# Optimization experiments

Measured on AMD Instinct MI355X. Metric: run time of the kernel, lower is better.

Reference implementation:

```python
import jax, jax.numpy as jnp
import numpy as np


def setup_inputs() -> dict:
    key = jax.random.key(0)
    kq, kk, kv = jax.random.split(key, 3)
    B, H, S, D = 2, 8, 2048, 64
    Q = jax.random.normal(kq, (B, H, S, D), dtype=jnp.float32)
    K = jax.random.normal(kk, (B, 1, S, D), dtype=jnp.float32)
    V = jax.random.normal(kv, (B, 1, S, D), dtype=jnp.float32)
    return {"Q": Q, "K": K, "V": V}


def reference(Q, K, V):
    # Multi-query attention: K/V have a single shared head.
    D = Q.shape[-1]
    scale = 1.0 / jnp.sqrt(jnp.asarray(D, dtype=Q.dtype))
    Kh = K[:, 0]  # [B, S, D]
    Vh = V[:, 0]  # [B, S, D]
    # scores: [B, H, Sq, Sk]
    scores = jnp.einsum('bhqd,bkd->bhqk', Q, Kh) * scale
    probs = jax.nn.softmax(scores, axis=-1)
    out = jnp.einsum('bhqk,bkd->bhqd', probs, Vh)  # [B, H, S, D]
    return out
```

## Files before the change

### kernel.cpp

```cpp
#include <hip/hip_runtime.h>
#include <stdint.h>

typedef __attribute__((ext_vector_type(8)))  short    bf16x8;
typedef __attribute__((ext_vector_type(16))) float    f32x16;
typedef __attribute__((ext_vector_type(4)))  float    float4v;
typedef __attribute__((ext_vector_type(4)))  unsigned uint4v;

#define DEVINL static __device__ __forceinline__

#define B_  2
#define H_  8
#define S_  2048
#define D_  64
#define KVB 128
#define NKT (S_ / KVB)

DEVINL unsigned short f2bf(float f) {
  union { float f; unsigned u; } v; v.f = f;
  unsigned r = v.u + 0x7FFFu + ((v.u >> 16) & 1u);
  return (unsigned short)(r >> 16);
}

DEVINL unsigned pk2(float a, float b) {
  return (unsigned)f2bf(a) | ((unsigned)f2bf(b) << 16);
}

DEVINL void gload_lds16(const void* g, void* l) {
  __builtin_amdgcn_global_load_lds(
      (const __attribute__((address_space(1))) void*)g,
      (__attribute__((address_space(3))) void*)l, 16, 0, 0);
}

DEVINL bf16x8 frag_from_words(unsigned a, unsigned b, unsigned c, unsigned d) {
  union { unsigned u[4]; bf16x8 v; } x;
  x.u[0] = a; x.u[1] = b; x.u[2] = c; x.u[3] = d;
  return x.v;
}

#define CROW(r, hi) (((r) & 3) + 8 * ((r) >> 2) + 4 * (hi))

__global__ __launch_bounds__(256) void prep_kernel(
    const float* __restrict__ K, const float* __restrict__ V,
    unsigned short* __restrict__ Kb, unsigned short* __restrict__ Vt) {
  const int t = threadIdx.x;
  if (blockIdx.x < 128) {
    const int base = blockIdx.x * 2048 + t * 8;
    const float4v a = *(const float4v*)(K + base);
    const float4v b = *(const float4v*)(K + base + 4);
    uint4v o;
    o.x = (unsigned)f2bf(a.x) | ((unsigned)f2bf(a.y) << 16);
    o.y = (unsigned)f2bf(a.z) | ((unsigned)f2bf(a.w) << 16);
    o.z = (unsigned)f2bf(b.x) | ((unsigned)f2bf(b.y) << 16);
    o.w = (unsigned)f2bf(b.z) | ((unsigned)f2bf(b.w) << 16);
    *(uint4v*)(Kb + base) = o;
  } else {
    __shared__ float Vf[64][65];
    const int vb   = blockIdx.x - 128;
    const int b    = vb >> 5;
    const int sblk = vb & 31;
    const int r = t >> 2, c = t & 3;
    const float* src = V + ((size_t)(b * S_ + sblk * 64 + r)) * 64 + c * 16;
#pragma unroll
    for (int j = 0; j < 4; ++j) {
      float4v x = *(const float4v*)(src + 4 * j);
      Vf[r][c * 16 + 4 * j + 0] = x.x;
      Vf[r][c * 16 + 4 * j + 1] = x.y;
      Vf[r][c * 16 + 4 * j + 2] = x.z;
      Vf[r][c * 16 + 4 * j + 3] = x.w;
    }
    __syncthreads();
    unsigned short o[16];
#pragma unroll
    for (int j = 0; j < 16; ++j) o[j] = f2bf(Vf[c * 16 + j][r]);
    unsigned short* dst = Vt + ((size_t)(b * 64 + r)) * S_ + sblk * 64 + c * 16;
    uint4v w0, w1;
    w0.x = (unsigned)o[0]  | ((unsigned)o[1]  << 16);
    w0.y = (unsigned)o[2]  | ((unsigned)o[3]  << 16);
    w0.z = (unsigned)o[4]  | ((unsigned)o[5]  << 16);
    w0.w = (unsigned)o[6]  | ((unsigned)o[7]  << 16);
    w1.x = (unsigned)o[8]  | ((unsigned)o[9]  << 16);
    w1.y = (unsigned)o[10] | ((unsigned)o[11] << 16);
    w1.z = (unsigned)o[12] | ((unsigned)o[13] << 16);
    w1.w = (unsigned)o[14] | ((unsigned)o[15] << 16);
    *(uint4v*)(dst)     = w0;
    *(uint4v*)(dst + 8) = w1;
  }
}

__global__ __launch_bounds__(256, 2) void attn_kernel(
    const float* __restrict__ Q, const unsigned short* __restrict__ Kb,
    const unsigned short* __restrict__ Vt, float* __restrict__ O) {
  __shared__ __align__(16) unsigned char smem[65536];

  const int bid = blockIdx.x;
  const int b  = bid >> 8;
  const int h  = (bid >> 5) & 7;
  const int qt = bid & 31;

  const int tid  = threadIdx.x;
  const int lane = tid & 63;
  const int wave = tid >> 6;
  const int qg   = wave & 1;
  const int kh   = wave >> 1;
  const int hi   = lane >> 5;
  const int lq   = lane & 31;
  const int l7   = lane & 7;

  const unsigned short* Kbase = Kb + (size_t)b * (S_ * 64);
  const unsigned short* Vbase = Vt + (size_t)b * (64 * S_);

  const float qscale = 0.125f * 1.4426950408889634f;
  const float* qrow = Q + ((size_t)((b * H_ + h) * S_) + (size_t)(qt * 64 + qg * 32 + lq)) * 64;
  bf16x8 qfrag[4];
#pragma unroll
  for (int ks = 0; ks < 4; ++ks) {
    const float* p = qrow + ks * 16 + hi * 8;
    float4v x0 = *(const float4v*)(p);
    float4v x1 = *(const float4v*)(p + 4);
    bf16x8 f;
    f[0] = (short)f2bf(x0.x * qscale); f[1] = (short)f2bf(x0.y * qscale);
    f[2] = (short)f2bf(x0.z * qscale); f[3] = (short)f2bf(x0.w * qscale);
    f[4] = (short)f2bf(x1.x * qscale); f[5] = (short)f2bf(x1.y * qscale);
    f[6] = (short)f2bf(x1.z * qscale); f[7] = (short)f2bf(x1.w * qscale);
    qfrag[ks] = f;
  }

  const int krow   = lane >> 3;
  const int kchunk = (lane & 7) ^ krow;
  const int vrow   = lane >> 4;

  f32x16 acc0, acc1;
#pragma unroll
  for (int r = 0; r < 16; ++r) { acc0[r] = 0.f; acc1[r] = 0.f; }
  float mrun = -__builtin_inff();
  float lrun = 0.f;

#define KL(BUF) ((unsigned short*)(smem + (BUF) * 16384))
#define VL(BUF) ((unsigned short*)(smem + 32768 + (BUF) * 16384))

#define STAGE(BUF, KT)                                                                   \
  do {                                                                                   \
    _Pragma("unroll")                                                                    \
    for (int i = 0; i < 4; ++i) {                                                        \
      const int kj = wave * 4 + i;                           \
      gload_lds16(Kbase + (size_t)((KT) * KVB + kj * 8 + krow) * 64 + kchunk * 8,        \
                  KL(BUF) + kj * 512 + lane * 8);                                        \
      const int vj = wave * 4 + i;                         \
      const int vr = vj * 4 + vrow;                                                      \
      const int vch = (lane & 15) ^ (vr & 7);                                            \
      gload_lds16(Vbase + (size_t)vr * S_ + (KT) * KVB + vch * 8,                        \
                  VL(BUF) + vj * 512 + lane * 8);                                        \
    }                                                                                    \
  } while (0)

  STAGE(0, 0);

  int buf = 0;
  for (int kt = 0; kt < NKT; ++kt) {
    __syncthreads();

    if (kt + 1 < NKT) STAGE(buf ^ 1, kt + 1);

    f32x16 c0, c1;
#pragma unroll
    for (int r = 0; r < 16; ++r) { c0[r] = 0.f; c1[r] = 0.f; }
    const unsigned short* Kt = KL(buf);
    __builtin_amdgcn_s_setprio(1);
#pragma unroll
    for (int ks = 0; ks < 4; ++ks) {
      const int ch = (2 * ks + hi) ^ l7;
      const bf16x8 a0 = *(const bf16x8*)(Kt + (kh * 64 + lq) * 64 + ch * 8);
      c0 = __builtin_amdgcn_mfma_f32_32x32x16_bf16(a0, qfrag[ks], c0, 0, 0, 0);
      const bf16x8 a1 = *(const bf16x8*)(Kt + (kh * 64 + 32 + lq) * 64 + ch * 8);
      c1 = __builtin_amdgcn_mfma_f32_32x32x16_bf16(a1, qfrag[ks], c1, 0, 0, 0);
    }
    __builtin_amdgcn_s_setprio(0);

    float mx = fmaxf(c0[0], c0[1]);
#pragma unroll
    for (int r = 2; r < 16; ++r) mx = fmaxf(mx, c0[r]);
#pragma unroll
    for (int r = 0; r < 16; ++r) mx = fmaxf(mx, c1[r]);
    mx = fmaxf(mx, __shfl_xor(mx, 32));

    if (!__all(mx <= mrun + 8.f)) {
      const float mnew = fmaxf(mrun, mx);
      const float fac  = __builtin_amdgcn_exp2f(mrun - mnew);
#pragma unroll
      for (int r = 0; r < 16; ++r) {
        const float fr = __shfl(fac, CROW(r, hi));
        acc0[r] *= fr; acc1[r] *= fr;
      }
      lrun *= fac;
      mrun = mnew;
    }

    float psum = 0.f;
#pragma unroll
    for (int r = 0; r < 16; ++r) {
      c0[r] = __builtin_amdgcn_exp2f(c0[r] - mrun);
      c1[r] = __builtin_amdgcn_exp2f(c1[r] - mrun);
      psum += c0[r] + c1[r];
    }
    psum += __shfl_xor(psum, 32);
    lrun += psum;

    const unsigned short* Vb = VL(buf);
#pragma unroll
    for (int ks = 0; ks < 4; ++ks) {
      const int e = ks & 1;
      const f32x16 ct = (ks >> 1) ? c1 : c0;
      const unsigned wx0 = pk2(ct[8 * e + 0], ct[8 * e + 1]);
      const unsigned wx1 = pk2(ct[8 * e + 2], ct[8 * e + 3]);
      const unsigned wy0 = pk2(ct[8 * e + 4], ct[8 * e + 5]);
      const unsigned wy1 = pk2(ct[8 * e + 6], ct[8 * e + 7]);
      const unsigned s0 = hi ? wx0 : wy0;
      const unsigned s1 = hi ? wx1 : wy1;
      const unsigned r0 = (unsigned)__shfl_xor((int)s0, 32);
      const unsigned r1 = (unsigned)__shfl_xor((int)s1, 32);
      const bf16x8 pfrag = frag_from_words(hi ? r0 : wx0, hi ? r1 : wx1,
                                           hi ? wy0 : r0, hi ? wy1 : r1);
      const int ch = (kh * 8) | ((2 * ks + hi) ^ l7);
      __builtin_amdgcn_s_setprio(1);
      const bf16x8 bv0 = *(const bf16x8*)(Vb + (size_t)lq * 128 + ch * 8);
      acc0 = __builtin_amdgcn_mfma_f32_32x32x16_bf16(pfrag, bv0, acc0, 0, 0, 0);
      const bf16x8 bv1 = *(const bf16x8*)(Vb + (size_t)(32 + lq) * 128 + ch * 8);
      acc1 = __builtin_amdgcn_mfma_f32_32x32x16_bf16(pfrag, bv1, acc1, 0, 0, 0);
      __builtin_amdgcn_s_setprio(0);
    }

    buf ^= 1;
  }

  __syncthreads();
  float* Mbuf = (float*)(smem + 16384);
  float* Lbuf = (float*)(smem + 16384 + 512);
  float* Abuf = (float*)(smem + 32768);
  if (lane < 32) {
    Mbuf[(qg * 2 + kh) * 32 + lane] = mrun;
    Lbuf[(qg * 2 + kh) * 32 + lane] = lrun;
  }
  __syncthreads();
  const float mo = Mbuf[(qg * 2 + (kh ^ 1)) * 32 + lq];
  const float lo = Lbuf[(qg * 2 + (kh ^ 1)) * 32 + lq];
  const float mtot  = fmaxf(mrun, mo);
  const float sself = __builtin_amdgcn_exp2f(mrun - mtot);
  const float ltot  = lrun * sself + lo * __builtin_amdgcn_exp2f(mo - mtot);

  if (kh == 1) {
#pragma unroll
    for (int r = 0; r < 16; ++r) {
      const float sr = __shfl(sself, CROW(r, hi));
      Abuf[qg * 2048 + CROW(r, hi) * 64 + lq]      = acc0[r] * sr;
      Abuf[qg * 2048 + CROW(r, hi) * 64 + 32 + lq] = acc1[r] * sr;
    }
  }
  __syncthreads();
  if (kh == 0) {
    const float linv = 1.f / ltot;
    float* obase = O + ((size_t)((b * H_ + h) * S_) + (size_t)(qt * 64 + qg * 32)) * 64;
#pragma unroll
    for (int r = 0; r < 16; ++r) {
      const float sr = __shfl(sself, CROW(r, hi));
      const float iv = __shfl(linv,  CROW(r, hi));
      const int row  = CROW(r, hi);
      obase[(size_t)row * 64 + lq]      = (acc0[r] * sr + Abuf[qg * 2048 + row * 64 + lq]) * iv;
      obase[(size_t)row * 64 + 32 + lq] = (acc1[r] * sr + Abuf[qg * 2048 + row * 64 + 32 + lq]) * iv;
    }
  }
}

extern "C" void kernel_launch(void* const* d_in, const int* in_sizes, int n_in,
                              void* d_out, int out_size, void* d_ws, size_t ws_size,
                              hipStream_t stream) {
  const float* Q = (const float*)d_in[0];
  const float* K = (const float*)d_in[1];
  const float* V = (const float*)d_in[2];
  float* O = (float*)d_out;

  unsigned short* Kb = (unsigned short*)d_ws;
  unsigned short* Vt = Kb + (size_t)B_ * S_ * 64;

  prep_kernel<<<192, 256, 0, stream>>>(K, V, Kb, Vt);
  attn_kernel<<<B_ * H_ * (S_ / 64), 256, 0, stream>>>(Q, Kb, Vt, O);
}
```

Baseline: 47.10 us.

## Use permlane32_swap, hardware bf16 convert, packed max/sum, and incremental staging pointers

Replaces the two shfl_xor plus select exchange of P fragments with gfx950 permlane32_swap instructions. Switches the manual round-to-nearest bf16 packing to the HIP __float2bfloat16 conversion, which may lower to the native convert. Vectorizes the row max and sum reductions into float2 packed operations. Precomputes the K/V staging pointers once and advances them each tile instead of recomputing addresses. All four aim to cut VALU and address work inside the inner loop, at the risk of the swap semantics or the staging layout not matching the previous per-lane mapping.

```diff
diff --git a/kernel.cpp b/kernel.cpp
--- a/kernel.cpp
+++ b/kernel.cpp
@@ -1,10 +1,13 @@
 #include <hip/hip_runtime.h>
+#include <hip/hip_bf16.h>
 #include <stdint.h>
 
 typedef __attribute__((ext_vector_type(8)))  short    bf16x8;
 typedef __attribute__((ext_vector_type(16))) float    f32x16;
+typedef __attribute__((ext_vector_type(2)))  float    f32x2;
 typedef __attribute__((ext_vector_type(4)))  float    float4v;
 typedef __attribute__((ext_vector_type(4)))  unsigned uint4v;
+typedef __attribute__((ext_vector_type(2)))  int      int2v;
 
 #define DEVINL static __device__ __forceinline__
 
@@ -21,8 +24,13 @@
   return (unsigned short)(r >> 16);
 }
 
-DEVINL unsigned pk2(float a, float b) {
-  return (unsigned)f2bf(a) | ((unsigned)f2bf(b) << 16);
+DEVINL unsigned short bfu(float f) {
+  __hip_bfloat16 h = __float2bfloat16(f);
+  unsigned short u; __builtin_memcpy(&u, &h, 2); return u;
+}
+
+DEVINL unsigned pkcvt(float a, float b) {
+  return (unsigned)bfu(a) | ((unsigned)bfu(b) << 16);
 }
 
 DEVINL void gload_lds16(const void* g, void* l) {
@@ -125,9 +133,14 @@
     qfrag[ks] = f;
   }
 
-  const int krow   = lane >> 3;
-  const int kchunk = (lane & 7) ^ krow;
-  const int vrow   = lane >> 4;
+  const int krow = lane >> 3;
+  const int kch  = (lane & 7) ^ krow;
+  const int vrow = lane >> 4;
+  const int vb0  = (lane & 15) ^ vrow;
+
+  const unsigned short* kp  = Kbase + (size_t)(wave * 32 + krow) * 64 + kch * 8;
+  const unsigned short* vpA = Vbase + (size_t)(wave * 16 + vrow) * S_ + vb0 * 8;
+  const unsigned short* vpB = Vbase + (size_t)(wave * 16 + vrow) * S_ + (vb0 ^ 4) * 8;
 
   f32x16 acc0, acc1;
 #pragma unroll
@@ -135,36 +148,30 @@
   float mrun = -__builtin_inff();
   float lrun = 0.f;
 
-#define KL(BUF) ((unsigned short*)(smem + (BUF) * 16384))
-#define VL(BUF) ((unsigned short*)(smem + 32768 + (BUF) * 16384))
-
-#define STAGE(BUF, KT)                                                                   \
+#define STAGE(BUF)                                                                       \
   do {                                                                                   \
     _Pragma("unroll")                                                                    \
     for (int i = 0; i < 4; ++i) {                                                        \
-      const int kj = wave * 4 + i;                           \
-      gload_lds16(Kbase + (size_t)((KT) * KVB + kj * 8 + krow) * 64 + kchunk * 8,        \
-                  KL(BUF) + kj * 512 + lane * 8);                                        \
-      const int vj = wave * 4 + i;                         \
-      const int vr = vj * 4 + vrow;                                                      \
-      const int vch = (lane & 15) ^ (vr & 7);                                            \
-      gload_lds16(Vbase + (size_t)vr * S_ + (KT) * KVB + vch * 8,                        \
-                  VL(BUF) + vj * 512 + lane * 8);                                        \
+      gload_lds16(kp + i * 512,                                                          \
+                  smem + (BUF) * 16384 + (wave * 4 + i) * 1024 + lane * 16);             \
+      gload_lds16(((i & 1) ? vpB : vpA) + i * 8192,                                      \
+                  smem + 32768 + (BUF) * 16384 + (wave * 4 + i) * 1024 + lane * 16);     \
     }                                                                                    \
+    kp += 8192; vpA += KVB; vpB += KVB;                                                  \
   } while (0)
 
-  STAGE(0, 0);
+  STAGE(0);
 
   int buf = 0;
   for (int kt = 0; kt < NKT; ++kt) {
     __syncthreads();
 
-    if (kt + 1 < NKT) STAGE(buf ^ 1, kt + 1);
+    if (kt + 1 < NKT) STAGE(buf ^ 1);
 
     f32x16 c0, c1;
 #pragma unroll
     for (int r = 0; r < 16; ++r) { c0[r] = 0.f; c1[r] = 0.f; }
-    const unsigned short* Kt = KL(buf);
+    const unsigned short* Kt = (const unsigned short*)(smem + buf * 16384);
     __builtin_amdgcn_s_setprio(1);
 #pragma unroll
     for (int ks = 0; ks < 4; ++ks) {
@@ -176,11 +183,14 @@
     }
     __builtin_amdgcn_s_setprio(0);
 
-    float mx = fmaxf(c0[0], c0[1]);
-#pragma unroll
-    for (int r = 2; r < 16; ++r) mx = fmaxf(mx, c0[r]);
-#pragma unroll
-    for (int r = 0; r < 16; ++r) mx = fmaxf(mx, c1[r]);
+    f32x2 m2 = (f32x2){c0[0], c0[1]};
+#pragma unroll
+    for (int r = 1; r < 8; ++r)
+      m2 = __builtin_elementwise_max(m2, (f32x2){c0[2 * r], c0[2 * r + 1]});
+#pragma unroll
+    for (int r = 0; r < 8; ++r)
+      m2 = __builtin_elementwise_max(m2, (f32x2){c1[2 * r], c1[2 * r + 1]});
+    float mx = fmaxf(m2.x, m2.y);
     mx = fmaxf(mx, __shfl_xor(mx, 32));
 
     if (!__all(mx <= mrun + 8.f)) {
@@ -195,31 +205,34 @@
       mrun = mnew;
     }
 
-    float psum = 0.f;
 #pragma unroll
     for (int r = 0; r < 16; ++r) {
       c0[r] = __builtin_amdgcn_exp2f(c0[r] - mrun);
       c1[r] = __builtin_amdgcn_exp2f(c1[r] - mrun);
-      psum += c0[r] + c1[r];
-    }
+    }
+    f32x2 ps = (f32x2){0.f, 0.f};
+#pragma unroll
+    for (int r = 0; r < 8; ++r) {
+      ps += (f32x2){c0[2 * r], c0[2 * r + 1]};
+      ps += (f32x2){c1[2 * r], c1[2 * r + 1]};
+    }
+    float psum = ps.x + ps.y;
     psum += __shfl_xor(psum, 32);
     lrun += psum;
 
-    const unsigned short* Vb = VL(buf);
+    const unsigned short* Vb = (const unsigned short*)(smem + 32768 + buf * 16384);
 #pragma unroll
     for (int ks = 0; ks < 4; ++ks) {
       const int e = ks & 1;
       const f32x16 ct = (ks >> 1) ? c1 : c0;
-      const unsigned wx0 = pk2(ct[8 * e + 0], ct[8 * e + 1]);
-      const unsigned wx1 = pk2(ct[8 * e + 2], ct[8 * e + 3]);
-      const unsigned wy0 = pk2(ct[8 * e + 4], ct[8 * e + 5]);
-      const unsigned wy1 = pk2(ct[8 * e + 6], ct[8 * e + 7]);
-      const unsigned s0 = hi ? wx0 : wy0;
-      const unsigned s1 = hi ? wx1 : wy1;
-      const unsigned r0 = (unsigned)__shfl_xor((int)s0, 32);
-      const unsigned r1 = (unsigned)__shfl_xor((int)s1, 32);
-      const bf16x8 pfrag = frag_from_words(hi ? r0 : wx0, hi ? r1 : wx1,
-                                           hi ? wy0 : r0, hi ? wy1 : r1);
+      const unsigned wx0 = pkcvt(ct[8 * e + 0], ct[8 * e + 1]);
+      const unsigned wx1 = pkcvt(ct[8 * e + 2], ct[8 * e + 3]);
+      const unsigned wy0 = pkcvt(ct[8 * e + 4], ct[8 * e + 5]);
+      const unsigned wy1 = pkcvt(ct[8 * e + 6], ct[8 * e + 7]);
+      const int2v s02 = __builtin_amdgcn_permlane32_swap((int)wx0, (int)wy0, false, false);
+      const int2v s13 = __builtin_amdgcn_permlane32_swap((int)wx1, (int)wy1, false, false);
+      const bf16x8 pfrag = frag_from_words((unsigned)s02.x, (unsigned)s13.x,
+                                           (unsigned)s02.y, (unsigned)s13.y);
       const int ch = (kh * 8) | ((2 * ks + hi) ^ l7);
       __builtin_amdgcn_s_setprio(1);
       const bf16x8 bv0 = *(const bf16x8*)(Vb + (size_t)lq * 128 + ch * 8);
```

Result: faster. 42.38 us (-10.0%).
